# Kernel optimization log

Measured on AMD Instinct MI355X. Metric: run time of the kernel, lower is better.

The kernel has to match this reference:

```python
import jax, jax.numpy as jnp
import numpy as np
import math

# AAMsoftmax constants (m=0.2, s=30), matching the torch implementation
M = 0.2
S = 30.0
COS_M = math.cos(M)
SIN_M = math.sin(M)
TH = math.cos(math.pi - M)
MM = math.sin(math.pi - M) * M

B, IN, P, C = 4096, 1024, 256, 5994


def _l2norm(v):
    # F.normalize: v / max(||v||, eps)
    n = jnp.sqrt(jnp.sum(v * v, axis=-1, keepdims=True))
    return v / jnp.maximum(n, 1e-12)


def setup_inputs() -> dict:
    key = jax.random.key(0)
    k0, k1, k2, k3 = jax.random.split(key, 4)
    return {
        "x": jax.random.normal(k0, (B, IN), jnp.float32),
        "label": jax.random.randint(k1, (B,), 0, C, dtype=jnp.int32),
        "W_fc": jax.random.normal(k2, (P, IN), jnp.float32) * (1.0 / np.sqrt(IN)),
        "b_fc": jnp.zeros((P,), jnp.float32),
        "W_aam": jax.random.normal(k3, (C, P), jnp.float32) * 0.05,
    }


def reference(x, label, W_fc, b_fc, W_aam):
    # fc layer: [B, IN] -> [B, P]
    e = x @ W_fc.T + b_fc
    # cosine similarity against class prototypes: [B, C]
    cosine = _l2norm(e) @ _l2norm(W_aam).T
    sine = jnp.sqrt(jnp.clip(1.0 - cosine * cosine, 0.0, 1.0))
    phi = cosine * COS_M - sine * SIN_M
    # easy-margin-off fallback: use cosine - mm where angle too large
    phi = jnp.where((cosine - TH) > 0, phi, cosine - MM)
    one_hot = jax.nn.one_hot(label, C, dtype=cosine.dtype)
    logits = (one_hot * phi + (1.0 - one_hot) * cosine) * S
    # cross-entropy (mean over batch)
    logp = jax.nn.log_softmax(logits, axis=-1)
    nll = -jnp.take_along_axis(logp, label[:, None].astype(jnp.int32), axis=1)[:, 0]
    return jnp.mean(nll)
```

## Files before the change

### kernel.cpp

```cpp
#include <hip/hip_runtime.h>
#include <math.h>

typedef __attribute__((ext_vector_type(8))) short bf16x8;
typedef __attribute__((ext_vector_type(4))) float f32x4;

#define AAM_COS_M 0.9800665778412416f
#define AAM_SIN_M 0.19866933079506122f
#define AAM_TH   (-0.9800665778412416f)
#define AAM_MM    0.03973386615901225f
#define C_CLS 5994

__device__ inline ushort f2bf(float f) {
    unsigned x = __float_as_uint(f);
    return (ushort)((x + 0x7fffu + ((x >> 16) & 1u)) >> 16);
}

__device__ __forceinline__ void gload16(const void* g, void* lds) {
    __builtin_amdgcn_global_load_lds(
        (const __attribute__((address_space(1))) unsigned int*)g,
        (__attribute__((address_space(3))) unsigned int*)lds, 16, 0, 0);
}

__global__ __launch_bounds__(256) void prep(const float* __restrict__ Wfc,
                                            const float* __restrict__ Waam,
                                            ushort* __restrict__ wfcb,
                                            ushort* __restrict__ Wn) {
    const int b = blockIdx.x;
    if (b < 256) {
        int i = b * 256 + threadIdx.x;
        float4 v = ((const float4*)Wfc)[i];
        ushort4 o;
        o.x = f2bf(v.x); o.y = f2bf(v.y); o.z = f2bf(v.z); o.w = f2bf(v.w);
        ((ushort4*)wfcb)[i] = o;
    } else {
        const int wave = threadIdx.x >> 6, lane = threadIdx.x & 63;
        const int row = (b - 256) * 4 + wave;
        ushort4 o;
        if (row < C_CLS) {
            float4 v = ((const float4*)&Waam[(size_t)row * 256])[lane];
            float ss = v.x * v.x + v.y * v.y + v.z * v.z + v.w * v.w;
#pragma unroll
            for (int m = 32; m >= 1; m >>= 1) ss += __shfl_xor(ss, m, 64);
            float sc = 1.f / fmaxf(sqrtf(ss), 1e-12f);
            o.x = f2bf(v.x * sc); o.y = f2bf(v.y * sc);
            o.z = f2bf(v.z * sc); o.w = f2bf(v.w * sc);
        } else {
            o.x = 0; o.y = 0; o.z = 0; o.w = 0;
        }
        ((ushort4*)&Wn[(size_t)row * 256])[lane] = o;
    }
}

__global__ __launch_bounds__(256) void fc_norm(const float* __restrict__ X,
                                               const ushort* __restrict__ Bm,
                                               const float* __restrict__ bias,
                                               ushort* __restrict__ En) {
    __shared__ float  Af[2][16 * 32];
    __shared__ ushort Bs[2][256 * 32];
    __shared__ float  red[4][16];
    const int tid = threadIdx.x, lane = tid & 63, w = tid >> 6;
    const int lx = lane & 15, lg = lane >> 4;
    const int rb = blockIdx.x * 16;

    const int arow = lane >> 3;
    const int agcol = ((lane & 7) ^ arow) * 4;
    const int brow = lane >> 2;
    const int bgcol = (((lane & 3) ^ (brow & 3)) * 8);

    f32x4 zero = {0.f, 0.f, 0.f, 0.f};
    f32x4 acc[4];
#pragma unroll
    for (int j = 0; j < 4; ++j) acc[j] = zero;

#define FC_STAGE(buf, k0) do {                                                  \
    if (w < 2)                                                                  \
        gload16(&X[(size_t)(rb + w * 8 + arow) * 1024 + (k0) + agcol],          \
                &Af[buf][w * 256]);                                             \
    _Pragma("unroll")                                                           \
    for (int s_ = 0; s_ < 4; ++s_) {                                            \
        int r0_ = w * 64 + s_ * 16;                                             \
        gload16(&Bm[(size_t)(r0_ + brow) * 1024 + (k0) + bgcol],                \
                &Bs[buf][r0_ * 32]);                                            \
    } } while (0)

    int cur = 0;
    FC_STAGE(0, 0);
    __syncthreads();

    for (int g = 0; g < 32; ++g) {
        if (g < 31) FC_STAGE(cur ^ 1, (g + 1) * 32);
        float4 fa0 = *(const float4*)&Af[cur][lx * 32 + (((lg * 2)     ^ (lx & 7)) * 4)];
        float4 fa1 = *(const float4*)&Af[cur][lx * 32 + (((lg * 2 + 1) ^ (lx & 7)) * 4)];
        bf16x8 af;
        af[0] = (short)f2bf(fa0.x); af[1] = (short)f2bf(fa0.y);
        af[2] = (short)f2bf(fa0.z); af[3] = (short)f2bf(fa0.w);
        af[4] = (short)f2bf(fa1.x); af[5] = (short)f2bf(fa1.y);
        af[6] = (short)f2bf(fa1.z); af[7] = (short)f2bf(fa1.w);
        bf16x8 bv[4];
#pragma unroll
        for (int j = 0; j < 4; ++j) {
            int rq = w * 64 + j * 16 + lx;
            bv[j] = *(const bf16x8*)&Bs[cur][rq * 32 + ((lg ^ (rq & 3)) * 8)];
        }
#pragma unroll
        for (int j = 0; j < 4; ++j)
            acc[j] = __builtin_amdgcn_mfma_f32_16x16x32_bf16(af, bv[j], acc[j], 0, 0, 0);
        __syncthreads();
        cur ^= 1;
    }
#undef FC_STAGE

    float v[4][4];
#pragma unroll
    for (int j = 0; j < 4; ++j) {
        float bb = bias[w * 64 + j * 16 + lx];
#pragma unroll
        for (int q = 0; q < 4; ++q) v[j][q] = acc[j][q] + bb;
    }
    float sq[4];
#pragma unroll
    for (int q = 0; q < 4; ++q) {
        float s = v[0][q] * v[0][q] + v[1][q] * v[1][q]
                + v[2][q] * v[2][q] + v[3][q] * v[3][q];
#pragma unroll
        for (int m = 8; m >= 1; m >>= 1) s += __shfl_xor(s, m, 64);
        sq[q] = s;
    }
    if (lx == 0) {
#pragma unroll
        for (int q = 0; q < 4; ++q) red[w][lg * 4 + q] = sq[q];
    }
    __syncthreads();
#pragma unroll
    for (int q = 0; q < 4; ++q) {
        int row = lg * 4 + q;
        float tot = red[0][row] + red[1][row] + red[2][row] + red[3][row];
        float sc = 1.f / fmaxf(sqrtf(tot), 1e-12f);
#pragma unroll
        for (int j = 0; j < 4; ++j)
            En[(size_t)(rb + row) * 256 + w * 64 + j * 16 + lx] = f2bf(v[j][q] * sc);
    }
}

__global__ __launch_bounds__(256, 2) void aam_mfma(const ushort* __restrict__ A,
                                                   const ushort* __restrict__ Bm,
                                                   const int* __restrict__ lab,
                                                   float* __restrict__ ps,
                                                   float* __restrict__ cosl) {
    __shared__ ushort As[2][128 * 64];
    __shared__ ushort Bs[2][128 * 64];
    const int tid = threadIdx.x, lane = tid & 63, w = tid >> 6;
    const int wr = w >> 1, wc = w & 1;
    const int lx = lane & 15, lg = lane >> 4;
    const int rb = blockIdx.x * 128;
    const int split = blockIdx.y;

    const int lrow = lane >> 3;
    const int gcol = ((lane & 7) ^ lrow) * 8;

    int labs[16];
#pragma unroll
    for (int idx = 0; idx < 16; ++idx)
        labs[idx] = lab[rb + wr * 64 + (idx >> 2) * 16 + lg * 4 + (idx & 3)];

    float srun[16];
#pragma unroll
    for (int idx = 0; idx < 16; ++idx) srun[idx] = 0.f;

    f32x4 zero = {0.f, 0.f, 0.f, 0.f};
    f32x4 acc[4][4];
#pragma unroll
    for (int i = 0; i < 4; ++i)
#pragma unroll
        for (int j = 0; j < 4; ++j) acc[i][j] = zero;

#define AAM_STAGE(buf, g) do {                                                  \
    int t_ = (g) >> 2, k0_ = ((g) & 3) * 64;                                    \
    int cb_ = split * 384 + t_ * 128;                                           \
    _Pragma("unroll")                                                           \
    for (int s_ = 0; s_ < 4; ++s_) {                                            \
        int r0_ = w * 32 + s_ * 8;                                              \
        gload16(&A[(size_t)(rb + r0_ + lrow) * 256 + k0_ + gcol],               \
                &As[buf][r0_ * 64]);                                            \
        gload16(&Bm[(size_t)(cb_ + r0_ + lrow) * 256 + k0_ + gcol],             \
                &Bs[buf][r0_ * 64]);                                            \
    } } while (0)

    int cur = 0;
    AAM_STAGE(0, 0);
    __syncthreads();

    for (int g = 0; g < 12; ++g) {
        if (g < 11) AAM_STAGE(cur ^ 1, g + 1);
#pragma unroll
        for (int kk = 0; kk < 2; ++kk) {
            bf16x8 af[4], bv[4];
#pragma unroll
            for (int f = 0; f < 4; ++f) {
                int ra = wr * 64 + f * 16 + lx;
                int ca = (lg + kk * 4) ^ (lx & 7);
                af[f] = *(const bf16x8*)&As[cur][ra * 64 + ca * 8];
                int rq = wc * 64 + f * 16 + lx;
                bv[f] = *(const bf16x8*)&Bs[cur][rq * 64 + ca * 8];
            }
#pragma unroll
            for (int i = 0; i < 4; ++i)
#pragma unroll
                for (int j = 0; j < 4; ++j)
                    acc[i][j] = __builtin_amdgcn_mfma_f32_16x16x32_bf16(af[i], bv[j], acc[i][j], 0, 0, 0);
        }
        if ((g & 3) == 3) {
            int cb_ = split * 384 + (g >> 2) * 128;
#pragma unroll
            for (int j = 0; j < 4; ++j) {
                int c = cb_ + wc * 64 + j * 16 + lx;
                if (c < C_CLS) {
#pragma unroll
                    for (int i = 0; i < 4; ++i)
#pragma unroll
                        for (int r = 0; r < 4; ++r) {
                            int idx = i * 4 + r;
                            float cosv = acc[i][j][r];
                            srun[idx] += __expf(30.f * cosv - 30.f);
                            if (c == labs[idx])
                                cosl[rb + wr * 64 + i * 16 + lg * 4 + r] = cosv;
                        }
                }
            }
#pragma unroll
            for (int i = 0; i < 4; ++i)
#pragma unroll
                for (int j = 0; j < 4; ++j) acc[i][j] = zero;
        }
        __syncthreads();
        cur ^= 1;
    }
#undef AAM_STAGE

#pragma unroll
    for (int idx = 0; idx < 16; ++idx) {
#pragma unroll
        for (int msk = 1; msk < 16; msk <<= 1)
            srun[idx] += __shfl_xor(srun[idx], msk, 64);
        if (lx == 0) {
            int row = rb + wr * 64 + (idx >> 2) * 16 + lg * 4 + (idx & 3);
            ps[(size_t)row * 32 + split * 2 + wc] = srun[idx];
        }
    }
}

__global__ __launch_bounds__(256) void reduce_nll(const float* __restrict__ ps,
                                                  const float* __restrict__ cosl,
                                                  float* __restrict__ partial) {
    __shared__ float red[4];
    const int row = blockIdx.x * 256 + threadIdx.x;
    const int wave = threadIdx.x >> 6, lane = threadIdx.x & 63;
    float s = 0.f;
#pragma unroll
    for (int q = 0; q < 8; ++q) {
        float4 v = ((const float4*)&ps[(size_t)row * 32])[q];
        s += v.x + v.y + v.z + v.w;
    }
    float cv = cosl[row];
    float sine = sqrtf(fmaxf(1.f - cv * cv, 0.f));
    float phi = cv * AAM_COS_M - sine * AAM_SIN_M;
    phi = ((cv - AAM_TH) > 0.f) ? phi : (cv - AAM_MM);
    float denom = s - __expf(30.f * cv - 30.f) + __expf(30.f * phi - 30.f);
    float nll = 30.f + logf(denom) - 30.f * phi;
#pragma unroll
    for (int m = 32; m >= 1; m >>= 1) nll += __shfl_xor(nll, m, 64);
    if (lane == 0) red[wave] = nll;
    __syncthreads();
    if (threadIdx.x == 0)
        partial[blockIdx.x] = red[0] + red[1] + red[2] + red[3];
}

__global__ __launch_bounds__(64) void final_reduce(const float* __restrict__ partial,
                                                   float* __restrict__ out) {
    const int lane = threadIdx.x;
    float v = (lane < 16) ? partial[lane] : 0.f;
#pragma unroll
    for (int m = 32; m >= 1; m >>= 1) v += __shfl_xor(v, m, 64);
    if (lane == 0) out[0] = v * (1.f / 4096.f);
}

extern "C" void kernel_launch(void* const* d_in, const int* in_sizes, int n_in,
                              void* d_out, int out_size, void* d_ws, size_t ws_size,
                              hipStream_t stream) {
    const float* x    = (const float*)d_in[0];
    const int*   lab  = (const int*)d_in[1];
    const float* Wfc  = (const float*)d_in[2];
    const float* bfc  = (const float*)d_in[3];
    const float* Waam = (const float*)d_in[4];
    float* out = (float*)d_out;

    char* ws = (char*)d_ws;
    ushort* En   = (ushort*)(ws);
    ushort* Wfcb = (ushort*)(ws + 2097152);
    ushort* Wn   = (ushort*)(ws + 2621440);
    float*  ps   = (float*) (ws + 5767168);
    float*  cosl = (float*) (ws + 6291456);
    float*  part = (float*) (ws + 6307840);

    prep<<<1792, 256, 0, stream>>>(Wfc, Waam, Wfcb, Wn);
    fc_norm<<<256, 256, 0, stream>>>(x, Wfcb, bfc, En);
    aam_mfma<<<dim3(32, 16), 256, 0, stream>>>(En, Wn, lab, ps, cosl);
    reduce_nll<<<16, 256, 0, stream>>>(ps, cosl, part);
    final_reduce<<<1, 64, 0, stream>>>(part, out);
}
```

Before: 128.4 us.

## Merge W_aam normalization into FC kernel and enlarge FC GEMM tiles

Moves the W_aam row-normalization out of the prep kernel and into extra blocks of the FC kernel (blocks 128-255), so it runs alongside the FC GEMM instead of serializing before it. The FC GEMM now uses 32-row by 64-wide K tiles, with two MFMA row fragments per wave, halving the number of blocks and K iterations and improving B-tile reuse. The fp32-to-bf16 conversion of X switches from round-to-nearest to truncation, which is cheaper but less accurate. The workspace layout is shuffled so Wfcb and En still fit before Wn. Fewer FC blocks (128) may underfill the GPU's compute units.

Result: faster. 122.0 us (-5.0%).

```diff
diff --git a/kernel.cpp b/kernel.cpp
--- a/kernel.cpp
+++ b/kernel.cpp
@@ -22,124 +22,144 @@
 }
 
 __global__ __launch_bounds__(256) void prep(const float* __restrict__ Wfc,
-                                            const float* __restrict__ Waam,
-                                            ushort* __restrict__ wfcb,
-                                            ushort* __restrict__ Wn) {
-    const int b = blockIdx.x;
-    if (b < 256) {
-        int i = b * 256 + threadIdx.x;
-        float4 v = ((const float4*)Wfc)[i];
-        ushort4 o;
-        o.x = f2bf(v.x); o.y = f2bf(v.y); o.z = f2bf(v.z); o.w = f2bf(v.w);
-        ((ushort4*)wfcb)[i] = o;
-    } else {
-        const int wave = threadIdx.x >> 6, lane = threadIdx.x & 63;
-        const int row = (b - 256) * 4 + wave;
-        ushort4 o;
-        if (row < C_CLS) {
-            float4 v = ((const float4*)&Waam[(size_t)row * 256])[lane];
-            float ss = v.x * v.x + v.y * v.y + v.z * v.z + v.w * v.w;
-#pragma unroll
-            for (int m = 32; m >= 1; m >>= 1) ss += __shfl_xor(ss, m, 64);
-            float sc = 1.f / fmaxf(sqrtf(ss), 1e-12f);
-            o.x = f2bf(v.x * sc); o.y = f2bf(v.y * sc);
-            o.z = f2bf(v.z * sc); o.w = f2bf(v.w * sc);
-        } else {
-            o.x = 0; o.y = 0; o.z = 0; o.w = 0;
-        }
-        ((ushort4*)&Wn[(size_t)row * 256])[lane] = o;
-    }
-}
-
-__global__ __launch_bounds__(256) void fc_norm(const float* __restrict__ X,
-                                               const ushort* __restrict__ Bm,
-                                               const float* __restrict__ bias,
-                                               ushort* __restrict__ En) {
-    __shared__ float  Af[2][16 * 32];
-    __shared__ ushort Bs[2][256 * 32];
-    __shared__ float  red[4][16];
+                                            ushort* __restrict__ wfcb) {
+    int i = blockIdx.x * 256 + threadIdx.x;
+    float4 v = ((const float4*)Wfc)[i];
+    ushort4 o;
+    o.x = f2bf(v.x); o.y = f2bf(v.y); o.z = f2bf(v.z); o.w = f2bf(v.w);
+    ((ushort4*)wfcb)[i] = o;
+}
+
+__global__ __launch_bounds__(256) void fcw(const float* __restrict__ X,
+                                           const ushort* __restrict__ Bm,
+                                           const float* __restrict__ bias,
+                                           const float* __restrict__ Waam,
+                                           ushort* __restrict__ En,
+                                           ushort* __restrict__ Wn) {
+    __shared__ float  Af[2][32 * 64];
+    __shared__ ushort Bs[2][256 * 64];
+    __shared__ float  red[4][32];
     const int tid = threadIdx.x, lane = tid & 63, w = tid >> 6;
+
+    if (blockIdx.x >= 128) {
+        const int base = (blockIdx.x - 128) * 48 + w * 12;
+        for (int r = 0; r < 12; ++r) {
+            const int row = base + r;
+            ushort4 o;
+            if (row < C_CLS) {
+                float4 v = ((const float4*)&Waam[(size_t)row * 256])[lane];
+                float ss = v.x * v.x + v.y * v.y + v.z * v.z + v.w * v.w;
+#pragma unroll
+                for (int m = 32; m >= 1; m >>= 1) ss += __shfl_xor(ss, m, 64);
+                float sc = 1.f / fmaxf(sqrtf(ss), 1e-12f);
+                o.x = f2bf(v.x * sc); o.y = f2bf(v.y * sc);
+                o.z = f2bf(v.z * sc); o.w = f2bf(v.w * sc);
+            } else {
+                o.x = 0; o.y = 0; o.z = 0; o.w = 0;
+            }
+            ((ushort4*)&Wn[(size_t)row * 256])[lane] = o;
+        }
+        return;
+    }
+
     const int lx = lane & 15, lg = lane >> 4;
-    const int rb = blockIdx.x * 16;
-
-    const int arow = lane >> 3;
-    const int agcol = ((lane & 7) ^ arow) * 4;
-    const int brow = lane >> 2;
-    const int bgcol = (((lane & 3) ^ (brow & 3)) * 8);
+    const int rb = blockIdx.x * 32;
 
     f32x4 zero = {0.f, 0.f, 0.f, 0.f};
-    f32x4 acc[4];
-#pragma unroll
-    for (int j = 0; j < 4; ++j) acc[j] = zero;
-
-#define FC_STAGE(buf, k0) do {                                                  \
-    if (w < 2)                                                                  \
-        gload16(&X[(size_t)(rb + w * 8 + arow) * 1024 + (k0) + agcol],          \
-                &Af[buf][w * 256]);                                             \
-    _Pragma("unroll")                                                           \
-    for (int s_ = 0; s_ < 4; ++s_) {                                            \
-        int r0_ = w * 64 + s_ * 16;                                             \
-        gload16(&Bm[(size_t)(r0_ + brow) * 1024 + (k0) + bgcol],                \
-                &Bs[buf][r0_ * 32]);                                            \
+    f32x4 acc[2][4];
+#pragma unroll
+    for (int i = 0; i < 2; ++i)
+#pragma unroll
+        for (int j = 0; j < 4; ++j) acc[i][j] = zero;
+
+#define FCW_STAGE(buf, k0) do {                                                \
+    _Pragma("unroll")                                                          \
+    for (int g_ = 0; g_ < 2; ++g_) {                                           \
+        int r_ = w * 8 + g_ * 4 + (lane >> 4);                                 \
+        int gc_ = ((lane & 15) ^ (r_ & 15)) * 4;                               \
+        gload16(&X[(size_t)(rb + r_) * 1024 + (k0) + gc_],                     \
+                &Af[buf][(w * 8 + g_ * 4) * 64]);                              \
+    }                                                                          \
+    _Pragma("unroll")                                                          \
+    for (int s_ = 0; s_ < 8; ++s_) {                                           \
+        int r_ = w * 64 + s_ * 8 + (lane >> 3);                                \
+        int gc_ = ((lane & 7) ^ (r_ & 7)) * 8;                                 \
+        gload16(&Bm[(size_t)r_ * 1024 + (k0) + gc_],                           \
+                &Bs[buf][(w * 64 + s_ * 8) * 64]);                             \
     } } while (0)
 
     int cur = 0;
-    FC_STAGE(0, 0);
+    FCW_STAGE(0, 0);
     __syncthreads();
 
-    for (int g = 0; g < 32; ++g) {
-        if (g < 31) FC_STAGE(cur ^ 1, (g + 1) * 32);
-        float4 fa0 = *(const float4*)&Af[cur][lx * 32 + (((lg * 2)     ^ (lx & 7)) * 4)];
-        float4 fa1 = *(const float4*)&Af[cur][lx * 32 + (((lg * 2 + 1) ^ (lx & 7)) * 4)];
-        bf16x8 af;
-        af[0] = (short)f2bf(fa0.x); af[1] = (short)f2bf(fa0.y);
-        af[2] = (short)f2bf(fa0.z); af[3] = (short)f2bf(fa0.w);
-        af[4] = (short)f2bf(fa1.x); af[5] = (short)f2bf(fa1.y);
-        af[6] = (short)f2bf(fa1.z); af[7] = (short)f2bf(fa1.w);
-        bf16x8 bv[4];
-#pragma unroll
-        for (int j = 0; j < 4; ++j) {
-            int rq = w * 64 + j * 16 + lx;
-            bv[j] = *(const bf16x8*)&Bs[cur][rq * 32 + ((lg ^ (rq & 3)) * 8)];
-        }
-#pragma unroll
-        for (int j = 0; j < 4; ++j)
-            acc[j] = __builtin_amdgcn_mfma_f32_16x16x32_bf16(af, bv[j], acc[j], 0, 0, 0);
+    for (int g = 0; g < 16; ++g) {
+        if (g < 15) FCW_STAGE(cur ^ 1, (g + 1) * 64);
+#pragma unroll
+        for (int kk = 0; kk < 2; ++kk) {
+            bf16x8 af[2];
+#pragma unroll
+            for (int i = 0; i < 2; ++i) {
+                int ra = i * 16 + lx;
+                int s0 = kk * 8 + lg * 2;
+                float4 fa0 = *(const float4*)&Af[cur][ra * 64 + (((s0    ) ^ (ra & 15)) * 4)];
+                float4 fa1 = *(const float4*)&Af[cur][ra * 64 + (((s0 + 1) ^ (ra & 15)) * 4)];
+                af[i][0] = (short)(__float_as_uint(fa0.x) >> 16);
+                af[i][1] = (short)(__float_as_uint(fa0.y) >> 16);
+                af[i][2] = (short)(__float_as_uint(fa0.z) >> 16);
+                af[i][3] = (short)(__float_as_uint(fa0.w) >> 16);
+                af[i][4] = (short)(__float_as_uint(fa1.x) >> 16);
+                af[i][5] = (short)(__float_as_uint(fa1.y) >> 16);
+                af[i][6] = (short)(__float_as_uint(fa1.z) >> 16);
+                af[i][7] = (short)(__float_as_uint(fa1.w) >> 16);
+            }
+            bf16x8 bv[4];
+#pragma unroll
+            for (int j = 0; j < 4; ++j) {
+                int rq = w * 64 + j * 16 + lx;
+                bv[j] = *(const bf16x8*)&Bs[cur][rq * 64 + (((kk * 4 + lg) ^ (rq & 7)) * 8)];
+            }
+#pragma unroll
+            for (int i = 0; i < 2; ++i)
+#pragma unroll
+                for (int j = 0; j < 4; ++j)
+                    acc[i][j] = __builtin_amdgcn_mfma_f32_16x16x32_bf16(af[i], bv[j], acc[i][j], 0, 0, 0);
+        }
         __syncthreads();
         cur ^= 1;
     }
-#undef FC_STAGE
-
-    float v[4][4];
+#undef FCW_STAGE
+
+    float v[2][4][4];
 #pragma unroll
     for (int j = 0; j < 4; ++j) {
         float bb = bias[w * 64 + j * 16 + lx];
 #pragma unroll
-        for (int q = 0; q < 4; ++q) v[j][q] = acc[j][q] + bb;
-    }
-    float sq[4];
-#pragma unroll
-    for (int q = 0; q < 4; ++q) {
-        float s = v[0][q] * v[0][q] + v[1][q] * v[1][q]
-                + v[2][q] * v[2][q] + v[3][q] * v[3][q];
-#pragma unroll
-        for (int m = 8; m >= 1; m >>= 1) s += __shfl_xor(s, m, 64);
-        sq[q] = s;
-    }
-    if (lx == 0) {
-#pragma unroll
-        for (int q = 0; q < 4; ++q) red[w][lg * 4 + q] = sq[q];
-    }
+        for (int i = 0; i < 2; ++i)
+#pragma unroll
+            for (int q = 0; q < 4; ++q) v[i][j][q] = acc[i][j][q] + bb;
+    }
+#pragma unroll
+    for (int i = 0; i < 2; ++i)
+#pragma unroll
+        for (int q = 0; q < 4; ++q) {
+            float s = v[i][0][q] * v[i][0][q] + v[i][1][q] * v[i][1][q]
+                    + v[i][2][q] * v[i][2][q] + v[i][3][q] * v[i][3][q];
+#pragma unroll
+            for (int m = 8; m >= 1; m >>= 1) s += __shfl_xor(s, m, 64);
+            if (lx == 0) red[w][i * 16 + lg * 4 + q] = s;
+        }
     __syncthreads();
 #pragma unroll
-    for (int q = 0; q < 4; ++q) {
-        int row = lg * 4 + q;
-        float tot = red[0][row] + red[1][row] + red[2][row] + red[3][row];
-        float sc = 1.f / fmaxf(sqrtf(tot), 1e-12f);
-#pragma unroll
-        for (int j = 0; j < 4; ++j)
-            En[(size_t)(rb + row) * 256 + w * 64 + j * 16 + lx] = f2bf(v[j][q] * sc);
-    }
+    for (int i = 0; i < 2; ++i)
+#pragma unroll
+        for (int q = 0; q < 4; ++q) {
+            int row = i * 16 + lg * 4 + q;
+            float tot = red[0][row] + red[1][row] + red[2][row] + red[3][row];
+            float sc = 1.f / fmaxf(sqrtf(tot), 1e-12f);
+#pragma unroll
+            for (int j = 0; j < 4; ++j)
+                En[(size_t)(rb + row) * 256 + w * 64 + j * 16 + lx] = f2bf(v[i][j][q] * sc);
+        }
 }
 
 __global__ __launch_bounds__(256, 2) void aam_mfma(const ushort* __restrict__ A,
@@ -295,15 +315,15 @@
     float* out = (float*)d_out;
 
     char* ws = (char*)d_ws;
-    ushort* En   = (ushort*)(ws);
-    ushort* Wfcb = (ushort*)(ws + 2097152);
+    ushort* Wfcb = (ushort*)(ws);
+    ushort* En   = (ushort*)(ws + 524288);
     ushort* Wn   = (ushort*)(ws + 2621440);
     float*  ps   = (float*) (ws + 5767168);
     float*  cosl = (float*) (ws + 6291456);
     float*  part = (float*) (ws + 6307840);
 
-    prep<<<1792, 256, 0, stream>>>(Wfc, Waam, Wfcb, Wn);
-    fc_norm<<<256, 256, 0, stream>>>(x, Wfcb, bfc, En);
+    prep<<<256, 256, 0, stream>>>(Wfc, Wfcb);
+    fcw<<<256, 256, 0, stream>>>(x, Wfcb, bfc, Waam, En, Wn);
     aam_mfma<<<dim3(32, 16), 256, 0, stream>>>(En, Wn, lab, ps, cosl);
     reduce_nll<<<16, 256, 0, stream>>>(ps, cosl, part);
     final_reduce<<<1, 64, 0, stream>>>(part, out);
```
